# Optimization experiments

Hardware: AMD Instinct MI355X
Metric: run time of the kernel (lower is better)

## Reference

```python
import jax, jax.numpy as jnp
import numpy as np

NUM_BITS = 10
MEM_SIZE = 2 ** NUM_BITS  # 1024
HIDDEN = 1024
INPUT = 1024
BATCH = 16384
LN_EPS = 1e-5


def setup_inputs() -> dict:
    key = jax.random.key(0)
    ks = jax.random.split(key, 8)
    s = 0.02
    return {
        "x": jax.random.normal(ks[0], (BATCH, INPUT), jnp.float32),
        "h_prev": jax.random.normal(ks[1], (BATCH, HIDDEN), jnp.float32),
        "memory": jax.random.normal(ks[2], (MEM_SIZE, HIDDEN), jnp.float32),
        "W_w": jax.random.normal(ks[3], (HIDDEN, INPUT), jnp.float32) * s,
        "W_b": jnp.zeros((HIDDEN,), jnp.float32),
        "U_w": jax.random.normal(ks[4], (HIDDEN, HIDDEN), jnp.float32) * s,
        "U_b": jnp.zeros((HIDDEN,), jnp.float32),
        "Q_w": jax.random.normal(ks[5], (HIDDEN, HIDDEN), jnp.float32) * s,
        "Q_b": jnp.zeros((HIDDEN,), jnp.float32),
        "M_w": jax.random.normal(ks[6], (NUM_BITS, HIDDEN), jnp.float32) * s,
        "M_b": jnp.zeros((NUM_BITS,), jnp.float32),
        "ln_g": jnp.ones((HIDDEN,), jnp.float32),
        "ln_b": jnp.zeros((HIDDEN,), jnp.float32),
    }


def reference(x, h_prev, memory, W_w, W_b, U_w, U_b, Q_w, Q_b, M_w, M_b, ln_g, ln_b):
    # Binary address from h_prev (eval-mode hard threshold, non-differentiable)
    powers = jnp.asarray(2 ** np.arange(NUM_BITS - 1, -1, -1), dtype=x.dtype)  # [num_bits]
    logits = h_prev @ M_w.T + M_b                              # [B, num_bits]
    binary = (jax.nn.sigmoid(logits) > 0.5).astype(x.dtype)    # hard bits
    index = jnp.clip((binary * powers).sum(-1).astype(jnp.int32), 0, MEM_SIZE - 1)  # [B]
    h_mem = memory[index]                                      # gather [B, H]
    # Fused linear combine + LayerNorm + sigmoid
    pre = x @ W_w.T + W_b + h_prev @ U_w.T + U_b + h_mem @ Q_w.T + Q_b  # [B, H]
    mu = pre.mean(-1, keepdims=True)
    var = ((pre - mu) ** 2).mean(-1, keepdims=True)            # biased var (torch LN)
    norm = (pre - mu) * jax.lax.rsqrt(var + LN_EPS)
    return jax.nn.sigmoid(norm * ln_g + ln_b)                  # h_new [B, H]
```

## Files before the change

### kernel.cpp

```cpp
#include <hip/hip_runtime.h>

#define BATCH   16384
#define HIDDEN  1024
#define K2      2048
#define MEMSZ   1024
#define NBITS   10

#define BM 256
#define BN 256
#define BK 64
#define NT (K2 / BK)

typedef __bf16 bf16x8 __attribute__((ext_vector_type(8)));
typedef float  f32x4  __attribute__((ext_vector_type(4)));
typedef unsigned short u16x8 __attribute__((ext_vector_type(8)));

__device__ __forceinline__ unsigned short f2bf(float f) {
    unsigned int u = __float_as_uint(f);
    u += 0x7FFFu + ((u >> 16) & 1u);
    return (unsigned short)(u >> 16);
}

__device__ __forceinline__ u16x8 f2bf8(float4 a, float4 b) {
    u16x8 r;
    r[0] = f2bf(a.x); r[1] = f2bf(a.y); r[2] = f2bf(a.z); r[3] = f2bf(a.w);
    r[4] = f2bf(b.x); r[5] = f2bf(b.y); r[6] = f2bf(b.z); r[7] = f2bf(b.w);
    return r;
}

__device__ __forceinline__ void gload_lds16(const void* g, void* l) {
    __builtin_amdgcn_global_load_lds(
        (const __attribute__((address_space(1))) unsigned int*)g,
        (__attribute__((address_space(3))) unsigned int*)l,
        16, 0, 0);
}

__global__ __launch_bounds__(256) void pack_build_kernel(
        const float* __restrict__ W, const float* __restrict__ U,
        const float* __restrict__ memory, const float* __restrict__ Q,
        const float* __restrict__ x, const float* __restrict__ h_prev,
        const float* __restrict__ M_w, const float* __restrict__ M_b,
        unsigned short* __restrict__ Bm, unsigned short* __restrict__ Mem,
        unsigned short* __restrict__ Qb, unsigned short* __restrict__ A,
        int* __restrict__ idxbuf) {
    if (blockIdx.x < 10240) {
        int u = blockIdx.x * 256 + threadIdx.x;
        const float* src;
        unsigned short* dst;
        if (u < 262144) {
            int n  = u >> 8;
            int k8 = (u & 255) << 3;
            src = (k8 < 1024) ? (W + (size_t)n * 1024 + k8)
                              : (U + (size_t)n * 1024 + (k8 - 1024));
            dst = Bm + (size_t)n * K2 + k8;
        } else if (u < 393216) {
            int f = (u - 262144) << 3;
            src = memory + f;  dst = Mem + f;
        } else if (u < 524288) {
            int f = (u - 393216) << 3;
            src = Q + f;  dst = Qb + f;
        } else {
            int e = (u - 524288) << 3;
            int row = e >> 10, col = e & 1023;
            src = x + (size_t)row * HIDDEN + col;
            dst = A + (size_t)row * K2 + col;
        }
        float4 a = *reinterpret_cast<const float4*>(src);
        float4 b = *reinterpret_cast<const float4*>(src + 4);
        *reinterpret_cast<u16x8*>(dst) = f2bf8(a, b);
        return;
    }

    const int row  = (blockIdx.x - 10240) * 4 + (threadIdx.x >> 6);
    const int lane = threadIdx.x & 63;

    const float* hr = h_prev + (size_t)row * HIDDEN;
    float4 hA0 = *reinterpret_cast<const float4*>(hr + lane * 8);
    float4 hA1 = *reinterpret_cast<const float4*>(hr + lane * 8 + 4);
    float4 hB0 = *reinterpret_cast<const float4*>(hr + 512 + lane * 8);
    float4 hB1 = *reinterpret_cast<const float4*>(hr + 512 + lane * 8 + 4);

    int idx = 0;
#pragma unroll
    for (int j = 0; j < NBITS; ++j) {
        const float* mp = M_w + (size_t)j * HIDDEN;
        float4 mA0 = *reinterpret_cast<const float4*>(mp + lane * 8);
        float4 mA1 = *reinterpret_cast<const float4*>(mp + lane * 8 + 4);
        float4 mB0 = *reinterpret_cast<const float4*>(mp + 512 + lane * 8);
        float4 mB1 = *reinterpret_cast<const float4*>(mp + 512 + lane * 8 + 4);
        float s = (hA0.x * mA0.x + hA0.y * mA0.y + hA0.z * mA0.z + hA0.w * mA0.w)
                + (hA1.x * mA1.x + hA1.y * mA1.y + hA1.z * mA1.z + hA1.w * mA1.w)
                + (hB0.x * mB0.x + hB0.y * mB0.y + hB0.z * mB0.z + hB0.w * mB0.w)
                + (hB1.x * mB1.x + hB1.y * mB1.y + hB1.z * mB1.z + hB1.w * mB1.w);
#pragma unroll
        for (int off = 32; off >= 1; off >>= 1) s += __shfl_xor(s, off, 64);
        if (s + M_b[j] > 0.f) idx |= 1 << (NBITS - 1 - j);
    }
    if (lane == 0) idxbuf[row] = idx;

    unsigned short* arow = A + (size_t)row * K2;
    *reinterpret_cast<u16x8*>(arow + 1024 + lane * 8) = f2bf8(hA0, hA1);
    *reinterpret_cast<u16x8*>(arow + 1536 + lane * 8) = f2bf8(hB0, hB1);
}

__global__ __launch_bounds__(256) void mq_kernel(
        const unsigned short* __restrict__ Mem,
        const unsigned short* __restrict__ Qb,
        float* __restrict__ MQ) {
    __shared__ unsigned short As[128 * 64];
    __shared__ unsigned short Bs[128 * 64];

    const int mb = blockIdx.x >> 3;
    const int nb = blockIdx.x & 7;
    const int t    = threadIdx.x;
    const int lane = t & 63;
    const int w    = t >> 6;
    const int wr   = w >> 1, wc = w & 1;
    const int rr   = lane & 15, rq = lane >> 4;
    const int c8   = (t & 7) * 8;
    const int srow = t >> 3;

    f32x4 acc[4][4] = {};

    for (int kt = 0; kt < 16; ++kt) {
        const int k0 = kt * 64;
#pragma unroll
        for (int i = 0; i < 4; ++i) {
            int r = i * 32 + srow;
            gload_lds16(Mem + (size_t)(mb * 128 + r) * 1024 + k0 + c8, As + i * 2048 + t * 8);
            gload_lds16(Qb  + (size_t)(nb * 128 + r) * 1024 + k0 + c8, Bs + i * 2048 + t * 8);
        }
        __syncthreads();
#pragma unroll
        for (int kk = 0; kk < 2; ++kk) {
            const int krd = kk * 32 + rq * 8;
            bf16x8 af[4], bfv[4];
#pragma unroll
            for (int m = 0; m < 4; ++m)
                af[m] = *reinterpret_cast<const bf16x8*>(As + (wr * 64 + m * 16 + rr) * 64 + krd);
#pragma unroll
            for (int n = 0; n < 4; ++n)
                bfv[n] = *reinterpret_cast<const bf16x8*>(Bs + (wc * 64 + n * 16 + rr) * 64 + krd);
#pragma unroll
            for (int m = 0; m < 4; ++m)
#pragma unroll
                for (int n = 0; n < 4; ++n)
                    acc[m][n] = __builtin_amdgcn_mfma_f32_16x16x32_bf16(
                        af[m], bfv[n], acc[m][n], 0, 0, 0);
        }
        __syncthreads();
    }

#pragma unroll
    for (int m = 0; m < 4; ++m)
#pragma unroll
        for (int n = 0; n < 4; ++n) {
            int gcol = nb * 128 + wc * 64 + n * 16 + rr;
#pragma unroll
            for (int j = 0; j < 4; ++j) {
                int grow = mb * 128 + wr * 64 + m * 16 + rq * 4 + j;
                MQ[(size_t)grow * 1024 + gcol] = acc[m][n][j];
            }
        }
}


__device__ __forceinline__ void stage_g(const unsigned short* __restrict__ src,
                                        int rowbase, int kt, int g,
                                        unsigned short* ldsTile, int t) {
    const int o      = g * 8192 + t * 16;
    const int row    = o >> 7;
    const int inner  = o & 127;
    const int sinner = inner ^ ((row & 7) << 4);
    const char* gp = reinterpret_cast<const char*>(
                         src + (size_t)(rowbase + row) * K2 + kt * BK) + sinner;
    gload_lds16(gp, reinterpret_cast<char*>(ldsTile) + o);
}

__device__ __forceinline__ bf16x8 ldsfrag(const unsigned short* tile, int row,
                                          int kbyte_x_sw) {
    return *reinterpret_cast<const bf16x8*>(
        reinterpret_cast<const char*>(tile) + row * 128 + kbyte_x_sw);
}

#define PH_BAR()                                                     \
    do {                                                             \
        asm volatile("" ::: "memory");                               \
        __builtin_amdgcn_s_barrier();                                \
        asm volatile("" ::: "memory");                               \
    } while (0)

#define LGKM(N)                                                      \
    do {                                                             \
        asm volatile("s_waitcnt lgkmcnt(" #N ")" ::: "memory");      \
        __builtin_amdgcn_sched_barrier(0);                           \
    } while (0)

#define MFMA_Q(AF, BF, MB, NB)                                                 \
    {                                                                          \
        __builtin_amdgcn_s_setprio(1);                                         \
        _Pragma("unroll") for (int m_ = 0; m_ < 4; ++m_)                       \
        _Pragma("unroll") for (int n_ = 0; n_ < 2; ++n_)                       \
        _Pragma("unroll") for (int kk_ = 0; kk_ < 2; ++kk_)                    \
            acc[(MB) + m_][(NB) + n_] =                                        \
                __builtin_amdgcn_mfma_f32_16x16x32_bf16(                       \
                    AF[m_][kk_], BF[n_][kk_],                                  \
                    acc[(MB) + m_][(NB) + n_], 0, 0, 0);                       \
        __builtin_amdgcn_s_setprio(0);                                         \
    }

__global__ __launch_bounds__(512, 2) void gemm_kernel(
        const unsigned short* __restrict__ A,
        const unsigned short* __restrict__ Bm,
        float* __restrict__ C) {
    __shared__ alignas(16) unsigned short lds[2][2][BM * BK];

    const int bid  = blockIdx.x;
    const int wgid = (bid & 7) * 32 + (bid >> 3);
    const int mblk = wgid >> 2;
    const int nblk = wgid & 3;

    const int t    = threadIdx.x;
    const int lane = t & 63;
    const int w    = t >> 6;
    const int wr   = w >> 2;
    const int wc   = w & 3;
    const int rr   = lane & 15;
    const int rq   = lane >> 4;
    const int sw   = (rr & 7) << 4;
    const int rqb  = rq * 16;
    const int wrb  = wr * 128;
    const int wcb  = wc * 64;

    const int arow = mblk * BM;
    const int brow = nblk * BN;

    f32x4 acc[8][4] = {};

    {
#pragma unroll
        for (int g = 0; g < 4; ++g) stage_g(A,  arow, 0, g, &lds[0][0][0], t);
#pragma unroll
        for (int g = 0; g < 4; ++g) stage_g(Bm, brow, 0, g, &lds[0][1][0], t);
#pragma unroll
        for (int g = 0; g < 4; ++g) stage_g(Bm, brow, 1, g, &lds[1][1][0], t);
#pragma unroll
        for (int g = 0; g < 4; ++g) stage_g(A,  arow, 1, g, &lds[1][0][0], t);
        asm volatile("s_waitcnt vmcnt(8)" ::: "memory");
        asm volatile("" ::: "memory");
        __builtin_amdgcn_s_barrier();
    }

    bf16x8 af  [4][2];
    bf16x8 af2 [4][2];
    bf16x8 bfr01[2][2];
    bf16x8 bfr23[2][2];

#pragma unroll
    for (int m = 0; m < 4; ++m) {
        af[m][0] = ldsfrag(&lds[0][0][0], wrb + m * 16 + rr, (rqb) ^ sw);
        af[m][1] = ldsfrag(&lds[0][0][0], wrb + m * 16 + rr, (64 + rqb) ^ sw);
    }
#pragma unroll
    for (int n = 0; n < 2; ++n) {
        bfr01[n][0] = ldsfrag(&lds[0][1][0], wcb + n * 16 + rr, (rqb) ^ sw);
        bfr01[n][1] = ldsfrag(&lds[0][1][0], wcb + n * 16 + rr, (64 + rqb) ^ sw);
    }

    for (int kt = 0; kt < NT; ++kt) {
        const int c = kt & 1;
        const unsigned short* At  = &lds[c][0][0];
        const unsigned short* Bt  = &lds[c][1][0];
        const unsigned short* nxA = &lds[c ^ 1][0][0];
        const unsigned short* nxB = &lds[c ^ 1][1][0];
        unsigned short* curA = &lds[c][0][0];
        unsigned short* curB = &lds[c][1][0];
        const bool pf1 = (kt + 1 < NT);
        const bool pf2 = (kt + 2 < NT);

        PH_BAR();
#pragma unroll
        for (int n = 0; n < 2; ++n) {
            bfr23[n][0] = ldsfrag(Bt, wcb + 32 + n * 16 + rr, (rqb) ^ sw);
            bfr23[n][1] = ldsfrag(Bt, wcb + 32 + n * 16 + rr, (64 + rqb) ^ sw);
        }
        af2[0][0] = ldsfrag(At, wrb + 64 + rr, (rqb) ^ sw);
        af2[0][1] = ldsfrag(At, wrb + 64 + rr, (64 + rqb) ^ sw);
        LGKM(6);
        MFMA_Q(af, bfr01, 0, 0);

        PH_BAR();
#pragma unroll
        for (int m = 1; m < 4; ++m) {
            af2[m][0] = ldsfrag(At, wrb + 64 + m * 16 + rr, (rqb) ^ sw);
            af2[m][1] = ldsfrag(At, wrb + 64 + m * 16 + rr, (64 + rqb) ^ sw);
        }
        LGKM(8);
        MFMA_Q(af, bfr23, 0, 2);
        __builtin_amdgcn_sched_barrier(0);
        asm volatile("s_waitcnt vmcnt(0)" ::: "memory");
        asm volatile("" ::: "memory");

        PH_BAR();
        if (pf2) {
            stage_g(Bm, brow, kt + 2, 0, curB, t);
            stage_g(Bm, brow, kt + 2, 1, curB, t);
            stage_g(Bm, brow, kt + 2, 2, curB, t);
            stage_g(Bm, brow, kt + 2, 3, curB, t);
        }
        if (pf1) {
#pragma unroll
            for (int m = 0; m < 3; ++m) {
                af[m][0] = ldsfrag(nxA, wrb + m * 16 + rr, (rqb) ^ sw);
                af[m][1] = ldsfrag(nxA, wrb + m * 16 + rr, (64 + rqb) ^ sw);
            }
            LGKM(6);
        } else {
            LGKM(0);
        }
        MFMA_Q(af2, bfr01, 4, 0);

        PH_BAR();
        if (pf2) {
            stage_g(A, arow, kt + 2, 0, curA, t);
            stage_g(A, arow, kt + 2, 1, curA, t);
            stage_g(A, arow, kt + 2, 2, curA, t);
            stage_g(A, arow, kt + 2, 3, curA, t);
        }
        if (pf1) {
            af[3][0] = ldsfrag(nxA, wrb + 48 + rr, (rqb) ^ sw);
            af[3][1] = ldsfrag(nxA, wrb + 48 + rr, (64 + rqb) ^ sw);
#pragma unroll
            for (int n = 0; n < 2; ++n) {
                bfr01[n][0] = ldsfrag(nxB, wcb + n * 16 + rr, (rqb) ^ sw);
                bfr01[n][1] = ldsfrag(nxB, wcb + n * 16 + rr, (64 + rqb) ^ sw);
            }
        }
        MFMA_Q(af2, bfr23, 4, 2);
    }

#pragma unroll
    for (int mi = 0; mi < 8; ++mi) {
#pragma unroll
        for (int n = 0; n < 4; ++n) {
            const int gcol = nblk * BN + wcb + n * 16 + rr;
#pragma unroll
            for (int j = 0; j < 4; ++j) {
                const int grow = mblk * BM + wrb + mi * 16 + rq * 4 + j;
                C[(size_t)grow * HIDDEN + gcol] = acc[mi][n][j];
            }
        }
    }
}

__global__ __launch_bounds__(256) void ln_kernel(
        float* __restrict__ C,
        const int* __restrict__ idxbuf,
        const float* __restrict__ MQ,
        const float* __restrict__ W_b, const float* __restrict__ U_b,
        const float* __restrict__ Q_b, const float* __restrict__ ln_g,
        const float* __restrict__ ln_b) {
    const int row = blockIdx.x;
    const int t   = threadIdx.x;
    const int midx = idxbuf[row];
    float4* rowp = reinterpret_cast<float4*>(C + (size_t)row * HIDDEN);
    const float4* mqp = reinterpret_cast<const float4*>(MQ + (size_t)midx * HIDDEN);

    float4 p  = rowp[t];
    float4 mq = mqp[t];
    float4 bw = reinterpret_cast<const float4*>(W_b)[t];
    float4 bu = reinterpret_cast<const float4*>(U_b)[t];
    float4 bq = reinterpret_cast<const float4*>(Q_b)[t];
    p.x += mq.x + bw.x + bu.x + bq.x;
    p.y += mq.y + bw.y + bu.y + bq.y;
    p.z += mq.z + bw.z + bu.z + bq.z;
    p.w += mq.w + bw.w + bu.w + bq.w;

    float s  = p.x + p.y + p.z + p.w;
    float sq = p.x * p.x + p.y * p.y + p.z * p.z + p.w * p.w;
#pragma unroll
    for (int off = 32; off >= 1; off >>= 1) {
        s  += __shfl_xor(s,  off, 64);
        sq += __shfl_xor(sq, off, 64);
    }
    __shared__ float red[8];
    const int lane = t & 63, w = t >> 6;
    if (lane == 0) { red[w] = s; red[4 + w] = sq; }
    __syncthreads();
    const float S    = red[0] + red[1] + red[2] + red[3];
    const float SQ   = red[4] + red[5] + red[6] + red[7];
    const float mean = S * (1.0f / HIDDEN);
    const float var  = SQ * (1.0f / HIDDEN) - mean * mean;
    const float rstd = rsqrtf(var + 1e-5f);

    float4 g = reinterpret_cast<const float4*>(ln_g)[t];
    float4 b = reinterpret_cast<const float4*>(ln_b)[t];
    float4 o;
    o.x = 1.f / (1.f + __expf(-((p.x - mean) * rstd * g.x + b.x)));
    o.y = 1.f / (1.f + __expf(-((p.y - mean) * rstd * g.y + b.y)));
    o.z = 1.f / (1.f + __expf(-((p.z - mean) * rstd * g.z + b.z)));
    o.w = 1.f / (1.f + __expf(-((p.w - mean) * rstd * g.w + b.w)));
    rowp[t] = o;
}

extern "C" void kernel_launch(void* const* d_in, const int* in_sizes, int n_in,
                              void* d_out, int out_size, void* d_ws, size_t ws_size,
                              hipStream_t stream) {
    const float* x      = (const float*)d_in[0];
    const float* h_prev = (const float*)d_in[1];
    const float* memory = (const float*)d_in[2];
    const float* W_w    = (const float*)d_in[3];
    const float* W_b    = (const float*)d_in[4];
    const float* U_w    = (const float*)d_in[5];
    const float* U_b    = (const float*)d_in[6];
    const float* Q_w    = (const float*)d_in[7];
    const float* Q_b    = (const float*)d_in[8];
    const float* M_w    = (const float*)d_in[9];
    const float* M_b    = (const float*)d_in[10];
    const float* ln_g   = (const float*)d_in[11];
    const float* ln_b   = (const float*)d_in[12];

    char* ws = (char*)d_ws;
    unsigned short* A   = (unsigned short*)(ws);
    unsigned short* Bm  = (unsigned short*)(ws + 67108864);
    unsigned short* Mem = (unsigned short*)(ws + 71303168);
    unsigned short* Qb  = (unsigned short*)(ws + 73400320);
    float*          MQ  = (float*)         (ws + 75497472);
    int*            idx = (int*)           (ws + 79691776);
    float* pre = (float*)d_out;

    hipLaunchKernelGGL(pack_build_kernel, dim3(14336), dim3(256), 0, stream,
                       W_w, U_w, memory, Q_w, x, h_prev, M_w, M_b,
                       Bm, Mem, Qb, A, idx);
    hipLaunchKernelGGL(mq_kernel, dim3(64), dim3(256), 0, stream,
                       Mem, Qb, MQ);
    hipLaunchKernelGGL(gemm_kernel, dim3((BATCH / BM) * (HIDDEN / BN)), dim3(512), 0, stream,
                       A, Bm, pre);
    hipLaunchKernelGGL(ln_kernel, dim3(BATCH), dim3(256), 0, stream,
                       pre, idx, MQ, W_b, U_b, Q_b, ln_g, ln_b);
}
```

Measured before the change: 173.5 us.

## Store GEMM output as bf16, fuse memory/Q conversion into mq kernel, batch pack loads

The GEMM now writes its pre-activation output as bf16 into workspace, and the LayerNorm kernel reads that back, which halves the intermediate write and read traffic when the workspace is large enough. The mq kernel reads fp32 memory and Q directly and converts to bf16 into a swizzled LDS tile, so the separate conversion pass is gone. The pack kernel handles four elements per thread with the loads issued together, and the address-bit projection does all ten reductions at once. Rounding the pre-activations to bf16 adds error before the LayerNorm, and the faster path depends on the workspace size.

```diff
diff --git a/kernel.cpp b/kernel.cpp
--- a/kernel.cpp
+++ b/kernel.cpp
@@ -11,6 +11,12 @@
 #define BK 64
 #define NT (K2 / BK)
 
+#define U_BM    262144
+#define U_TOT   2359296
+#define SBLK    2304
+#define SSTRIDE (SBLK * 256)
+#define BBLK    4096
+
 typedef __bf16 bf16x8 __attribute__((ext_vector_type(8)));
 typedef float  f32x4  __attribute__((ext_vector_type(4)));
 typedef unsigned short u16x8 __attribute__((ext_vector_type(8)));
@@ -19,6 +25,10 @@
     unsigned int u = __float_as_uint(f);
     u += 0x7FFFu + ((u >> 16) & 1u);
     return (unsigned short)(u >> 16);
+}
+
+__device__ __forceinline__ float bf2f(unsigned short u) {
+    return __uint_as_float((unsigned int)u << 16);
 }
 
 __device__ __forceinline__ u16x8 f2bf8(float4 a, float4 b) {
@@ -28,6 +38,12 @@
     return r;
 }
 
+__device__ __forceinline__ ushort4 f2bf4(float4 a) {
+    ushort4 r;
+    r.x = f2bf(a.x); r.y = f2bf(a.y); r.z = f2bf(a.z); r.w = f2bf(a.w);
+    return r;
+}
+
 __device__ __forceinline__ void gload_lds16(const void* g, void* l) {
     __builtin_amdgcn_global_load_lds(
         (const __attribute__((address_space(1))) unsigned int*)g,
@@ -35,80 +51,93 @@
         16, 0, 0);
 }
 
-__global__ __launch_bounds__(256) void pack_build_kernel(
+__global__ __launch_bounds__(256, 8) void pre_kernel(
         const float* __restrict__ W, const float* __restrict__ U,
-        const float* __restrict__ memory, const float* __restrict__ Q,
         const float* __restrict__ x, const float* __restrict__ h_prev,
         const float* __restrict__ M_w, const float* __restrict__ M_b,
-        unsigned short* __restrict__ Bm, unsigned short* __restrict__ Mem,
-        unsigned short* __restrict__ Qb, unsigned short* __restrict__ A,
+        unsigned short* __restrict__ Bm, unsigned short* __restrict__ A,
         int* __restrict__ idxbuf) {
-    if (blockIdx.x < 10240) {
-        int u = blockIdx.x * 256 + threadIdx.x;
-        const float* src;
-        unsigned short* dst;
-        if (u < 262144) {
-            int n  = u >> 8;
-            int k8 = (u & 255) << 3;
-            src = (k8 < 1024) ? (W + (size_t)n * 1024 + k8)
-                              : (U + (size_t)n * 1024 + (k8 - 1024));
-            dst = Bm + (size_t)n * K2 + k8;
-        } else if (u < 393216) {
-            int f = (u - 262144) << 3;
-            src = memory + f;  dst = Mem + f;
-        } else if (u < 524288) {
-            int f = (u - 393216) << 3;
-            src = Q + f;  dst = Qb + f;
-        } else {
-            int e = (u - 524288) << 3;
-            int row = e >> 10, col = e & 1023;
-            src = x + (size_t)row * HIDDEN + col;
-            dst = A + (size_t)row * K2 + col;
-        }
-        float4 a = *reinterpret_cast<const float4*>(src);
-        float4 b = *reinterpret_cast<const float4*>(src + 4);
-        *reinterpret_cast<u16x8*>(dst) = f2bf8(a, b);
+    if (blockIdx.x < SBLK) {
+        const int u0 = blockIdx.x * 256 + threadIdx.x;
+        const float* s4[4];
+        unsigned short* d4[4];
+#pragma unroll
+        for (int i = 0; i < 4; ++i) {
+            int u = u0 + i * SSTRIDE;
+            if (u < U_BM) {
+                int n  = u >> 8;
+                int k8 = (u & 255) << 3;
+                s4[i] = (k8 < 1024) ? (W + (size_t)n * 1024 + k8)
+                                    : (U + (size_t)n * 1024 + (k8 - 1024));
+                d4[i] = Bm + (size_t)n * K2 + k8;
+            } else {
+                int e = (u - U_BM) << 3;
+                int row = e >> 10, col = e & 1023;
+                s4[i] = x + (size_t)row * HIDDEN + col;
+                d4[i] = A + (size_t)row * K2 + col;
+            }
+        }
+        float4 va[4], vb[4];
+#pragma unroll
+        for (int i = 0; i < 4; ++i) {
+            va[i] = *reinterpret_cast<const float4*>(s4[i]);
+            vb[i] = *reinterpret_cast<const float4*>(s4[i] + 4);
+        }
+        __builtin_amdgcn_sched_barrier(0);
+#pragma unroll
+        for (int i = 0; i < 4; ++i)
+            *reinterpret_cast<u16x8*>(d4[i]) = f2bf8(va[i], vb[i]);
         return;
     }
 
-    const int row  = (blockIdx.x - 10240) * 4 + (threadIdx.x >> 6);
+    const int bb   = blockIdx.x - SBLK;
+    const int wv   = threadIdx.x >> 6;
     const int lane = threadIdx.x & 63;
+    const int row  = bb * 4 + wv;
+    const int c4   = lane * 4;
 
     const float* hr = h_prev + (size_t)row * HIDDEN;
-    float4 hA0 = *reinterpret_cast<const float4*>(hr + lane * 8);
-    float4 hA1 = *reinterpret_cast<const float4*>(hr + lane * 8 + 4);
-    float4 hB0 = *reinterpret_cast<const float4*>(hr + 512 + lane * 8);
-    float4 hB1 = *reinterpret_cast<const float4*>(hr + 512 + lane * 8 + 4);
-
+    float4 h[4];
+#pragma unroll
+    for (int seg = 0; seg < 4; ++seg)
+        h[seg] = *reinterpret_cast<const float4*>(hr + seg * 256 + c4);
+
+    float s[NBITS];
+#pragma unroll
+    for (int j = 0; j < NBITS; ++j) {
+        const float* mj = M_w + (size_t)j * HIDDEN;
+        float4 m0 = *reinterpret_cast<const float4*>(mj + 0 * 256 + c4);
+        float4 m1 = *reinterpret_cast<const float4*>(mj + 1 * 256 + c4);
+        float4 m2 = *reinterpret_cast<const float4*>(mj + 2 * 256 + c4);
+        float4 m3 = *reinterpret_cast<const float4*>(mj + 3 * 256 + c4);
+        s[j] = (h[0].x * m0.x + h[0].y * m0.y + h[0].z * m0.z + h[0].w * m0.w)
+             + (h[1].x * m1.x + h[1].y * m1.y + h[1].z * m1.z + h[1].w * m1.w)
+             + (h[2].x * m2.x + h[2].y * m2.y + h[2].z * m2.z + h[2].w * m2.w)
+             + (h[3].x * m3.x + h[3].y * m3.y + h[3].z * m3.z + h[3].w * m3.w);
+    }
+#pragma unroll
+    for (int off = 32; off >= 1; off >>= 1) {
+#pragma unroll
+        for (int j = 0; j < NBITS; ++j) s[j] += __shfl_xor(s[j], off, 64);
+    }
     int idx = 0;
 #pragma unroll
-    for (int j = 0; j < NBITS; ++j) {
-        const float* mp = M_w + (size_t)j * HIDDEN;
-        float4 mA0 = *reinterpret_cast<const float4*>(mp + lane * 8);
-        float4 mA1 = *reinterpret_cast<const float4*>(mp + lane * 8 + 4);
-        float4 mB0 = *reinterpret_cast<const float4*>(mp + 512 + lane * 8);
-        float4 mB1 = *reinterpret_cast<const float4*>(mp + 512 + lane * 8 + 4);
-        float s = (hA0.x * mA0.x + hA0.y * mA0.y + hA0.z * mA0.z + hA0.w * mA0.w)
-                + (hA1.x * mA1.x + hA1.y * mA1.y + hA1.z * mA1.z + hA1.w * mA1.w)
-                + (hB0.x * mB0.x + hB0.y * mB0.y + hB0.z * mB0.z + hB0.w * mB0.w)
-                + (hB1.x * mB1.x + hB1.y * mB1.y + hB1.z * mB1.z + hB1.w * mB1.w);
-#pragma unroll
-        for (int off = 32; off >= 1; off >>= 1) s += __shfl_xor(s, off, 64);
-        if (s + M_b[j] > 0.f) idx |= 1 << (NBITS - 1 - j);
-    }
+    for (int j = 0; j < NBITS; ++j)
+        if (s[j] + M_b[j] > 0.f) idx |= 1 << (NBITS - 1 - j);
     if (lane == 0) idxbuf[row] = idx;
 
-    unsigned short* arow = A + (size_t)row * K2;
-    *reinterpret_cast<u16x8*>(arow + 1024 + lane * 8) = f2bf8(hA0, hA1);
-    *reinterpret_cast<u16x8*>(arow + 1536 + lane * 8) = f2bf8(hB0, hB1);
+    unsigned short* arow = A + (size_t)row * K2 + 1024;
+#pragma unroll
+    for (int seg = 0; seg < 4; ++seg)
+        *reinterpret_cast<ushort4*>(arow + seg * 256 + c4) = f2bf4(h[seg]);
 }
 
 __global__ __launch_bounds__(256) void mq_kernel(
-        const unsigned short* __restrict__ Mem,
-        const unsigned short* __restrict__ Qb,
+        const float* __restrict__ memory,
+        const float* __restrict__ Q,
         float* __restrict__ MQ) {
-    __shared__ unsigned short As[128 * 64];
-    __shared__ unsigned short Bs[128 * 64];
+    __shared__ unsigned short As[128 * 32];
+    __shared__ unsigned short Bs[128 * 32];
 
     const int mb = blockIdx.x >> 3;
     const int nb = blockIdx.x & 7;
@@ -117,38 +146,53 @@
     const int w    = t >> 6;
     const int wr   = w >> 1, wc = w & 1;
     const int rr   = lane & 15, rq = lane >> 4;
-    const int c8   = (t & 7) * 8;
-    const int srow = t >> 3;
+    const int srow = t >> 1;
+    const int scol = (t & 1) * 16;
+    const int swr  = (srow & 3) << 4;
 
     f32x4 acc[4][4] = {};
 
-    for (int kt = 0; kt < 16; ++kt) {
-        const int k0 = kt * 64;
-#pragma unroll
-        for (int i = 0; i < 4; ++i) {
-            int r = i * 32 + srow;
-            gload_lds16(Mem + (size_t)(mb * 128 + r) * 1024 + k0 + c8, As + i * 2048 + t * 8);
-            gload_lds16(Qb  + (size_t)(nb * 128 + r) * 1024 + k0 + c8, Bs + i * 2048 + t * 8);
-        }
+    for (int kt = 0; kt < 32; ++kt) {
+        const int k0 = kt * 32;
+        const float* ap = memory + (size_t)(mb * 128 + srow) * 1024 + k0 + scol;
+        const float* bp = Q      + (size_t)(nb * 128 + srow) * 1024 + k0 + scol;
+        float4 a0 = *reinterpret_cast<const float4*>(ap);
+        float4 a1 = *reinterpret_cast<const float4*>(ap + 4);
+        float4 a2 = *reinterpret_cast<const float4*>(ap + 8);
+        float4 a3 = *reinterpret_cast<const float4*>(ap + 12);
+        float4 b0 = *reinterpret_cast<const float4*>(bp);
+        float4 b1 = *reinterpret_cast<const float4*>(bp + 4);
+        float4 b2 = *reinterpret_cast<const float4*>(bp + 8);
+        float4 b3 = *reinterpret_cast<const float4*>(bp + 12);
         __syncthreads();
-#pragma unroll
-        for (int kk = 0; kk < 2; ++kk) {
-            const int krd = kk * 32 + rq * 8;
-            bf16x8 af[4], bfv[4];
-#pragma unroll
-            for (int m = 0; m < 4; ++m)
-                af[m] = *reinterpret_cast<const bf16x8*>(As + (wr * 64 + m * 16 + rr) * 64 + krd);
+        {
+            char* ar = reinterpret_cast<char*>(As) + srow * 64;
+            char* br = reinterpret_cast<char*>(Bs) + srow * 64;
+            *reinterpret_cast<u16x8*>(ar + ((scol * 2)      ^ swr)) = f2bf8(a0, a1);
+            *reinterpret_cast<u16x8*>(ar + ((scol * 2 + 16) ^ swr)) = f2bf8(a2, a3);
+            *reinterpret_cast<u16x8*>(br + ((scol * 2)      ^ swr)) = f2bf8(b0, b1);
+            *reinterpret_cast<u16x8*>(br + ((scol * 2 + 16) ^ swr)) = f2bf8(b2, b3);
+        }
+        __syncthreads();
+        bf16x8 af[4], bfv[4];
+#pragma unroll
+        for (int m = 0; m < 4; ++m) {
+            int r = wr * 64 + m * 16 + rr;
+            af[m] = *reinterpret_cast<const bf16x8*>(
+                reinterpret_cast<const char*>(As) + r * 64 + ((rq * 16) ^ ((r & 3) << 4)));
+        }
+#pragma unroll
+        for (int n = 0; n < 4; ++n) {
+            int r = wc * 64 + n * 16 + rr;
+            bfv[n] = *reinterpret_cast<const bf16x8*>(
+                reinterpret_cast<const char*>(Bs) + r * 64 + ((rq * 16) ^ ((r & 3) << 4)));
+        }
+#pragma unroll
+        for (int m = 0; m < 4; ++m)
 #pragma unroll
             for (int n = 0; n < 4; ++n)
-                bfv[n] = *reinterpret_cast<const bf16x8*>(Bs + (wc * 64 + n * 16 + rr) * 64 + krd);
-#pragma unroll
-            for (int m = 0; m < 4; ++m)
-#pragma unroll
-                for (int n = 0; n < 4; ++n)
-                    acc[m][n] = __builtin_amdgcn_mfma_f32_16x16x32_bf16(
-                        af[m], bfv[n], acc[m][n], 0, 0, 0);
-        }
-        __syncthreads();
+                acc[m][n] = __builtin_amdgcn_mfma_f32_16x16x32_bf16(
+                    af[m], bfv[n], acc[m][n], 0, 0, 0);
     }
 
 #pragma unroll
@@ -209,10 +253,11 @@
         __builtin_amdgcn_s_setprio(0);                                         \
     }
 
+template <bool BF16C>
 __global__ __launch_bounds__(512, 2) void gemm_kernel(
         const unsigned short* __restrict__ A,
         const unsigned short* __restrict__ Bm,
-        float* __restrict__ C) {
+        void* __restrict__ Cout) {
     __shared__ alignas(16) unsigned short lds[2][2][BM * BK];
 
     const int bid  = blockIdx.x;
@@ -347,14 +392,20 @@
 #pragma unroll
             for (int j = 0; j < 4; ++j) {
                 const int grow = mblk * BM + wrb + mi * 16 + rq * 4 + j;
-                C[(size_t)grow * HIDDEN + gcol] = acc[mi][n][j];
+                if constexpr (BF16C) {
+                    ((unsigned short*)Cout)[(size_t)grow * HIDDEN + gcol] =
+                        f2bf(acc[mi][n][j]);
+                } else {
+                    ((float*)Cout)[(size_t)grow * HIDDEN + gcol] = acc[mi][n][j];
+                }
             }
         }
     }
 }
 
+template <bool BF16C>
 __global__ __launch_bounds__(256) void ln_kernel(
-        float* __restrict__ C,
+        const void* __restrict__ Cin, float* __restrict__ out,
         const int* __restrict__ idxbuf,
         const float* __restrict__ MQ,
         const float* __restrict__ W_b, const float* __restrict__ U_b,
@@ -363,10 +414,17 @@
     const int row = blockIdx.x;
     const int t   = threadIdx.x;
     const int midx = idxbuf[row];
-    float4* rowp = reinterpret_cast<float4*>(C + (size_t)row * HIDDEN);
     const float4* mqp = reinterpret_cast<const float4*>(MQ + (size_t)midx * HIDDEN);
 
-    float4 p  = rowp[t];
+    float4 p;
+    if constexpr (BF16C) {
+        ushort4 uv = reinterpret_cast<const ushort4*>(
+            (const unsigned short*)Cin + (size_t)row * HIDDEN)[t];
+        p.x = bf2f(uv.x); p.y = bf2f(uv.y); p.z = bf2f(uv.z); p.w = bf2f(uv.w);
+    } else {
+        p = reinterpret_cast<const float4*>(
+            (const float*)Cin + (size_t)row * HIDDEN)[t];
+    }
     float4 mq = mqp[t];
     float4 bw = reinterpret_cast<const float4*>(W_b)[t];
     float4 bu = reinterpret_cast<const float4*>(U_b)[t];
@@ -400,7 +458,7 @@
     o.y = 1.f / (1.f + __expf(-((p.y - mean) * rstd * g.y + b.y)));
     o.z = 1.f / (1.f + __expf(-((p.z - mean) * rstd * g.z + b.z)));
     o.w = 1.f / (1.f + __expf(-((p.w - mean) * rstd * g.w + b.w)));
-    rowp[t] = o;
+    reinterpret_cast<float4*>(out + (size_t)row * HIDDEN)[t] = o;
 }
 
 extern "C" void kernel_launch(void* const* d_in, const int* in_sizes, int n_in,
@@ -423,19 +481,28 @@
     char* ws = (char*)d_ws;
     unsigned short* A   = (unsigned short*)(ws);
     unsigned short* Bm  = (unsigned short*)(ws + 67108864);
-    unsigned short* Mem = (unsigned short*)(ws + 71303168);
-    unsigned short* Qb  = (unsigned short*)(ws + 73400320);
-    float*          MQ  = (float*)         (ws + 75497472);
-    int*            idx = (int*)           (ws + 79691776);
+    float*          MQ  = (float*)         (ws + 71303168);
+    int*            idx = (int*)           (ws + 75497472);
+    unsigned short* Cb  = (unsigned short*)(ws + 75563008);
+    const bool bf16c = ws_size >= (size_t)75563008 + 33554432;
+
     float* pre = (float*)d_out;
 
-    hipLaunchKernelGGL(pack_build_kernel, dim3(14336), dim3(256), 0, stream,
-                       W_w, U_w, memory, Q_w, x, h_prev, M_w, M_b,
-                       Bm, Mem, Qb, A, idx);
+    hipLaunchKernelGGL(pre_kernel, dim3(SBLK + BBLK), dim3(256), 0, stream,
+                       W_w, U_w, x, h_prev, M_w, M_b, Bm, A, idx);
     hipLaunchKernelGGL(mq_kernel, dim3(64), dim3(256), 0, stream,
-                       Mem, Qb, MQ);
-    hipLaunchKernelGGL(gemm_kernel, dim3((BATCH / BM) * (HIDDEN / BN)), dim3(512), 0, stream,
-                       A, Bm, pre);
-    hipLaunchKernelGGL(ln_kernel, dim3(BATCH), dim3(256), 0, stream,
-                       pre, idx, MQ, W_b, U_b, Q_b, ln_g, ln_b);
-}
+                       memory, Q_w, MQ);
+    if (bf16c) {
+        hipLaunchKernelGGL((gemm_kernel<true>), dim3((BATCH / BM) * (HIDDEN / BN)),
+                           dim3(512), 0, stream, A, Bm, (void*)Cb);
+        hipLaunchKernelGGL((ln_kernel<true>), dim3(BATCH), dim3(256), 0, stream,
+                           (const void*)Cb, (float*)d_out, idx, MQ,
+                           W_b, U_b, Q_b, ln_g, ln_b);
+    } else {
+        hipLaunchKernelGGL((gemm_kernel<false>), dim3((BATCH / BM) * (HIDDEN / BN)),
+                           dim3(512), 0, stream, A, Bm, (void*)pre);
+        hipLaunchKernelGGL((ln_kernel<false>), dim3(BATCH), dim3(256), 0, stream,
+                           (const void*)pre, (float*)d_out, idx, MQ,
+                           W_b, U_b, Q_b, ln_g, ln_b);
+    }
+}
```

After: 255.1 us. 1.47x slower.
